# Kernel optimization log

Measured on AMD Instinct MI355X. Metric: run time of the kernel, lower is better.

## Reference

```python
import jax, jax.numpy as jnp
import numpy as np

V, E, L, H, B, T = 32000, 1024, 6, 16, 4, 1024
HS = E // H
FF = 4 * E


def setup_inputs() -> dict:
    key = jax.random.key(0)
    ks = jax.random.split(key, 16)
    s = 0.02
    n = lambda k, shp: jax.random.normal(k, shp, jnp.float32) * s
    return {
        "tokens": jax.random.randint(ks[0], (B, T), 0, V),
        "tok_emb": n(ks[1], (V, E)),
        "pos_emb": n(ks[2], (T, E)),
        "Wq": n(ks[3], (L, E, E)),
        "Wk": n(ks[4], (L, E, E)),
        "Wv": n(ks[5], (L, E, E)),
        "Wo": n(ks[6], (L, E, E)),
        "ln1_g": jnp.ones((L, E), jnp.float32),
        "ln1_b": jnp.zeros((L, E), jnp.float32),
        "W1": n(ks[7], (L, E, FF)),
        "b1": jnp.zeros((L, FF), jnp.float32),
        "W2": n(ks[8], (L, FF, E)),
        "b2": jnp.zeros((L, E), jnp.float32),
        "ln2_g": jnp.ones((L, E), jnp.float32),
        "ln2_b": jnp.zeros((L, E), jnp.float32),
        "lmh_w": n(ks[9], (E, V)),
        "lmh_b": jnp.zeros((V,), jnp.float32),
    }


def _layernorm(x, g, b):
    m = jnp.mean(x, axis=-1, keepdims=True)
    v = jnp.var(x, axis=-1, keepdims=True)
    return (x - m) * jax.lax.rsqrt(v + 1e-5) * g + b


def _forward(tokens, tok_emb, pos_emb, Wq, Wk, Wv, Wo, ln1_g, ln1_b,
             W1, b1, W2, b2, ln2_g, ln2_b, lmh_w, lmh_b):
    Bb, Tt = tokens.shape
    x = tok_emb[tokens] + pos_emb[:Tt]  # [B,T,E]
    mask = jnp.tril(jnp.ones((Tt, Tt), bool))  # causal
    scale = jnp.float32(E) ** -0.5  # NOTE: original scales by emb_dim, not head_size

    def block(x, p):
        wq, wk, wv, wo, g1, be1, w1, bb1, w2, bb2, g2, be2 = p
        h = _layernorm(x, g1, be1)
        q = (h @ wq).reshape(Bb, Tt, H, HS)
        k = (h @ wk).reshape(Bb, Tt, H, HS)
        v = (h @ wv).reshape(Bb, Tt, H, HS)
        scores = jnp.einsum('bqhd,bkhd->bhqk', q, k) * scale
        scores = jnp.where(mask, scores, -jnp.inf)
        w = jax.nn.softmax(scores, axis=-1)
        attn = jnp.einsum('bhqk,bkhd->bqhd', w, v).reshape(Bb, Tt, E)
        x = x + attn @ wo
        h2 = _layernorm(x, g2, be2)
        x = x + jax.nn.relu(h2 @ w1 + bb1) @ w2 + bb2
        return x, None

    x, _ = jax.lax.scan(block, x, (Wq, Wk, Wv, Wo, ln1_g, ln1_b,
                                   W1, b1, W2, b2, ln2_g, ln2_b))
    logits = x @ lmh_w + lmh_b  # [B,T,V]
    return logits


def reference(tokens, tok_emb, pos_emb, Wq, Wk, Wv, Wo, ln1_g, ln1_b,
              W1, b1, W2, b2, ln2_g, ln2_b, lmh_w, lmh_b):
    return _forward(tokens, tok_emb, pos_emb, Wq, Wk, Wv, Wo, ln1_g, ln1_b,
                    W1, b1, W2, b2, ln2_g, ln2_b, lmh_w, lmh_b)
```

## Files before the change

kernel.cpp:

```cpp
#include <hip/hip_runtime.h>
#include <cstdint>
#include <cstddef>

typedef __bf16 bf16;
typedef __attribute__((ext_vector_type(8))) __bf16 bf16x8;
typedef __attribute__((ext_vector_type(4))) float f32x4;

constexpr int kV = 32000, kE = 1024, kL = 6, kH = 16, kB = 4, kT = 1024;
constexpr int kHS = 64, kFF = 4096;
constexpr int kM = kB * kT;
constexpr float kScale = 0.03125f;
constexpr float kQScale = 0.0451038961f;

typedef __attribute__((address_space(1))) void gv_t;
typedef __attribute__((address_space(3))) void lv_t;

__device__ inline void gload_lds16(const void* g, void* l) {
  __builtin_amdgcn_global_load_lds((gv_t*)g, (lv_t*)l, 16, 0, 0);
}

#define SB0() __builtin_amdgcn_sched_barrier(0)
#define LGK0() asm volatile("s_waitcnt lgkmcnt(0)" ::: "memory")

enum { EPI_BF16 = 0, EPI_BF16_BIAS_RELU = 1, EPI_F32 = 2, EPI_F32_RES = 3, EPI_F32_BIAS = 4 };

__device__ inline void xcd_swz(int& bx, int& by) {
  int gx = gridDim.x, gy = gridDim.y;
  int nxy = gx * gy;
  int orig = by * gx + bx;
  int q = nxy >> 3, r = nxy & 7, xcd = orig & 7, idx = orig >> 3;
  int logical = (xcd < r ? xcd * (q + 1) : r * (q + 1) + (xcd - r) * q) + idx;
  bx = logical / gy;
  by = logical % gy;
}

template <int EPI>
__global__ __launch_bounds__(512, 2) void gemm256_k(
    const bf16* __restrict__ Ag, const bf16* __restrict__ Bg, void* Cg,
    const float* __restrict__ bias, const float* __restrict__ resid,
    int K, long lda, long ldb, long ldc) {
  extern __shared__ bf16 lds[];
  constexpr int SL = 8192;
  bf16* As = lds;
  bf16* Bs = lds + 4 * SL;

  const int tid = threadIdx.x, lane = tid & 63, w = tid >> 6;
  int bx = blockIdx.x, by = blockIdx.y;
  xcd_swz(bx, by);
  const long tm = (long)by * 256, tn = (long)bx * 256;
  const int wr = w >> 2, wc = w & 3;
  const int lr = lane & 15, kg = lane >> 4;

  const int p0 = tid, p1 = 512 + tid;
  const int r0 = p0 >> 2, ls0 = (p0 & 3) ^ ((r0 >> 1) & 3);
  const int r1 = p1 >> 2, ls1 = (p1 & 3) ^ ((r1 >> 1) & 3);
  const bf16* a0 = Ag + (tm + r0) * lda + ls0 * 8;
  const bf16* a1 = Ag + (tm + r1) * lda + ls1 * 8;
  const bf16* b0 = Bg + (tn + r0) * ldb + ls0 * 8;
  const bf16* b1 = Bg + (tn + r1) * ldb + ls1 * 8;
  const int wb = w * 1024;

  auto stage = [&](int s) {
    const int slot = s & 3;
    const long k0 = (long)s * 32;
    char* Ab = (char*)As + slot * (SL * 2);
    char* Bb = (char*)Bs + slot * (SL * 2);
    gload_lds16(a0 + k0, Ab + wb);
    gload_lds16(a1 + k0, Ab + 8192 + wb);
    gload_lds16(b0 + k0, Bb + wb);
    gload_lds16(b1 + k0, Bb + 8192 + wb);
  };

  int aoff[8], boff[4];
#pragma unroll
  for (int mi = 0; mi < 8; mi++) {
    int ar = wr * 128 + mi * 16 + lr;
    aoff[mi] = ar * 64 + ((kg ^ ((ar >> 1) & 3)) << 4);
  }
#pragma unroll
  for (int ni = 0; ni < 4; ni++) {
    int br = wc * 64 + ni * 16 + lr;
    boff[ni] = br * 64 + ((kg ^ ((br >> 1) & 3)) << 4);
  }

  f32x4 acc[8][4] = {};
  stage(0);
  stage(1);
  stage(2);
  const int NS = K >> 5;
  for (int s = 0; s < NS; s++) {
    SB0();
    if (s <= NS - 3)
      asm volatile("s_waitcnt vmcnt(8)" ::: "memory");
    else if (s == NS - 2)
      asm volatile("s_waitcnt vmcnt(4)" ::: "memory");
    else
      asm volatile("s_waitcnt vmcnt(0)" ::: "memory");
    __builtin_amdgcn_s_barrier();
    SB0();
    if (s + 3 < NS) stage(s + 3);
    const char* Ab = (const char*)As + (s & 3) * (SL * 2);
    const char* Bb = (const char*)Bs + (s & 3) * (SL * 2);
    bf16x8 af[8], bfr[4];
#pragma unroll
    for (int mi = 0; mi < 8; mi++) af[mi] = *(const bf16x8*)(Ab + aoff[mi]);
#pragma unroll
    for (int ni = 0; ni < 4; ni++) bfr[ni] = *(const bf16x8*)(Bb + boff[ni]);
    __builtin_amdgcn_s_setprio(1);
#pragma unroll
    for (int mi = 0; mi < 8; mi++)
#pragma unroll
      for (int ni = 0; ni < 4; ni++)
        acc[mi][ni] =
            __builtin_amdgcn_mfma_f32_16x16x32_bf16(af[mi], bfr[ni], acc[mi][ni], 0, 0, 0);
    __builtin_amdgcn_s_setprio(0);
  }

#pragma unroll
  for (int mi = 0; mi < 8; mi++) {
#pragma unroll
    for (int ni = 0; ni < 4; ni++) {
      const long rr = tm + wr * 128 + mi * 16 + kg * 4;
      const long cc = tn + wc * 64 + ni * 16 + lr;
      float bi = 0.f;
      if constexpr (EPI == EPI_BF16_BIAS_RELU || EPI == EPI_F32_BIAS) bi = bias[cc];
      if constexpr (EPI == EPI_F32_RES) bi = bias ? bias[cc] : 0.f;
#pragma unroll
      for (int j = 0; j < 4; j++) {
        long off = (rr + j) * ldc + cc;
        float val = acc[mi][ni][j];
        if constexpr (EPI == EPI_BF16)
          __builtin_nontemporal_store((bf16)val, &((bf16*)Cg)[off]);
        else if constexpr (EPI == EPI_BF16_BIAS_RELU)
          __builtin_nontemporal_store((bf16)fmaxf(val + bi, 0.f), &((bf16*)Cg)[off]);
        else if constexpr (EPI == EPI_F32)
          __builtin_nontemporal_store(val, &((float*)Cg)[off]);
        else if constexpr (EPI == EPI_F32_RES)
          ((float*)Cg)[off] = resid[off] + val + bi;
        else
          __builtin_nontemporal_store(val + bi, &((float*)Cg)[off]);
      }
    }
  }
}

template <int EPI>
__global__ __launch_bounds__(256, 2) void ring128_k(
    const bf16* __restrict__ Ag, const bf16* __restrict__ Bg, void* Cg,
    const float* __restrict__ bias, const float* __restrict__ resid,
    int K, long lda, long ldb, long ldc) {
  extern __shared__ bf16 lds[];
  char* Lb = (char*)lds;
  const int tid = threadIdx.x, lane = tid & 63, w = tid >> 6;
  int bx = blockIdx.x, by = blockIdx.y;
  xcd_swz(bx, by);
  const long tm = (long)by * 128, tn = (long)bx * 128;
  const int wr = w >> 1, wc = w & 1;
  const int lr = lane & 15, kg = lane >> 4;

  const int r0 = tid >> 2, g0 = (tid & 3) ^ ((r0 >> 1) & 3);
  const int r1 = (256 + tid) >> 2, g1 = ((256 + tid) & 3) ^ ((r1 >> 1) & 3);
  const bf16* a0 = Ag + (tm + r0) * lda + g0 * 8;
  const bf16* a1 = Ag + (tm + r1) * lda + g1 * 8;
  const bf16* b0 = Bg + (tn + r0) * ldb + g0 * 8;
  const bf16* b1 = Bg + (tn + r1) * ldb + g1 * 8;
  const int wb = w * 1024;

  auto stage = [&](int s) {
    const int slot = s & 3;
    const long k0 = (long)s * 32;
    char* Ab = Lb + slot * 16384;
    char* Bb = Ab + 8192;
    gload_lds16(a0 + k0, Ab + wb);
    gload_lds16(a1 + k0, Ab + 4096 + wb);
    gload_lds16(b0 + k0, Bb + wb);
    gload_lds16(b1 + k0, Bb + 4096 + wb);
  };

  int aoff[4], boff[4];
#pragma unroll
  for (int mi = 0; mi < 4; mi++) {
    int ar = wr * 64 + mi * 16 + lr;
    aoff[mi] = ar * 64 + ((kg ^ ((ar >> 1) & 3)) << 4);
  }
#pragma unroll
  for (int ni = 0; ni < 4; ni++) {
    int br = wc * 64 + ni * 16 + lr;
    boff[ni] = br * 64 + ((kg ^ ((br >> 1) & 3)) << 4);
  }

  f32x4 acc[4][4] = {};
  stage(0);
  stage(1);
  stage(2);
  const int NS = K >> 5;
  for (int s = 0; s < NS; s++) {
    SB0();
    if (s <= NS - 3)
      asm volatile("s_waitcnt vmcnt(8)" ::: "memory");
    else if (s == NS - 2)
      asm volatile("s_waitcnt vmcnt(4)" ::: "memory");
    else
      asm volatile("s_waitcnt vmcnt(0)" ::: "memory");
    __builtin_amdgcn_s_barrier();
    SB0();
    if (s + 3 < NS) stage(s + 3);
    const char* Ab = Lb + (s & 3) * 16384;
    const char* Bb = Ab + 8192;
    bf16x8 af[4], bfr[4];
#pragma unroll
    for (int mi = 0; mi < 4; mi++) af[mi] = *(const bf16x8*)(Ab + aoff[mi]);
#pragma unroll
    for (int ni = 0; ni < 4; ni++) bfr[ni] = *(const bf16x8*)(Bb + boff[ni]);
    __builtin_amdgcn_s_setprio(1);
#pragma unroll
    for (int mi = 0; mi < 4; mi++)
#pragma unroll
      for (int ni = 0; ni < 4; ni++)
        acc[mi][ni] =
            __builtin_amdgcn_mfma_f32_16x16x32_bf16(af[mi], bfr[ni], acc[mi][ni], 0, 0, 0);
    __builtin_amdgcn_s_setprio(0);
  }

#pragma unroll
  for (int mi = 0; mi < 4; mi++) {
#pragma unroll
    for (int ni = 0; ni < 4; ni++) {
      const long rr = tm + wr * 64 + mi * 16 + kg * 4;
      const long cc = tn + wc * 64 + ni * 16 + lr;
      float bi = 0.f;
      if constexpr (EPI == EPI_BF16_BIAS_RELU || EPI == EPI_F32_BIAS) bi = bias[cc];
      if constexpr (EPI == EPI_F32_RES) bi = bias ? bias[cc] : 0.f;
#pragma unroll
      for (int j = 0; j < 4; j++) {
        long off = (rr + j) * ldc + cc;
        float val = acc[mi][ni][j];
        if constexpr (EPI == EPI_BF16)
          ((bf16*)Cg)[off] = (bf16)val;
        else if constexpr (EPI == EPI_BF16_BIAS_RELU)
          ((bf16*)Cg)[off] = (bf16)fmaxf(val + bi, 0.f);
        else if constexpr (EPI == EPI_F32)
          ((float*)Cg)[off] = val;
        else if constexpr (EPI == EPI_F32_RES)
          ((float*)Cg)[off] = resid[off] + val + bi;
        else
          ((float*)Cg)[off] = val + bi;
      }
    }
  }
}

__global__ __launch_bounds__(128) void fa_k(const bf16* __restrict__ qkv,
                                            const bf16* __restrict__ vtG,
                                            bf16* __restrict__ out) {
  extern __shared__ bf16 lds[];
  char* L = (char*)lds;
  const int tid = threadIdx.x, lane = tid & 63, wq = tid >> 6;
  const int lr = lane & 15, kg = lane >> 4;
  const int bh = blockIdx.x, z = blockIdx.y;
  const int b = bh >> 4, hh = bh & 15;
  const long bq = (long)b * kT;
  const int qt = z < 4 ? z : 11 - z;
  const int q0 = qt * 128;
  const bf16* qbase = qkv + (bq + q0) * 3072 + hh * 64;
  const bf16* vbase = vtG + (long)bh * 64 * kT;

#pragma unroll
  for (int i = 0; i < 8; i++) {
    int p = i * 128 + tid;
    int row = p >> 3, s = p & 7;
    gload_lds16(qbase + (long)row * 3072 + ((s ^ (row & 7)) * 8),
                L + (i * 128 + (tid & ~63)) * 16);
  }
  auto stageKV = [&](int buf, int t) {
    const bf16* kb = qkv + (bq + t * 64) * 3072 + 1024 + hh * 64;
    const bf16* vb = vbase + t * 64;
#pragma unroll
    for (int i = 0; i < 4; i++) {
      int p = i * 128 + tid;
      int key = p >> 3, s = p & 7;
      gload_lds16(kb + (long)key * 3072 + ((s ^ (key & 7)) * 8),
                  L + 16384 + buf * 8192 + (i * 128 + (tid & ~63)) * 16);
    }
#pragma unroll
    for (int i = 0; i < 4; i++) {
      int p = i * 128 + tid;
      int key = p >> 3, s = p & 7;
      gload_lds16(vb + (long)key * kT + s * 8,
                  L + 32768 + buf * 8192 + (i * 128 + (tid & ~63)) * 16);
    }
  };
  stageKV(0, 0);
  __syncthreads();

  bf16x8 qf[4][2];
#pragma unroll
  for (int qi = 0; qi < 4; qi++)
#pragma unroll
    for (int ks = 0; ks < 2; ks++) {
      int qr = wq * 64 + qi * 16 + lr;
      bf16x8 v = *(const bf16x8*)(L + qr * 128 + ((ks * 64 + kg * 16) ^ ((qr & 7) << 4)));
#pragma unroll
      for (int e = 0; e < 8; e++) v[e] = (bf16)((float)v[e] * kQScale);
      qf[qi][ks] = v;
    }

  f32x4 O[4][4] = {};
  float lrun[4] = {0.f, 0.f, 0.f, 0.f};
  char* Pw = L + 49152 + wq * 9216;

  const int nt = 2 * qt + 2;
  int cur = 0;
  for (int t = 0; t < nt; t++) {
    if (t + 1 < nt) stageKV(cur ^ 1, t + 1);

    const char* Kb = L + 16384 + cur * 8192;
    f32x4 S[4][4] = {};
#pragma unroll
    for (int ks = 0; ks < 2; ks++) {
      bf16x8 kf[4];
#pragma unroll
      for (int ki = 0; ki < 4; ki++) {
        int key = ki * 16 + lr;
        kf[ki] = *(const bf16x8*)(Kb + key * 128 + ((ks * 64 + kg * 16) ^ ((key & 7) << 4)));
      }
#pragma unroll
      for (int ki = 0; ki < 4; ki++)
#pragma unroll
        for (int qi = 0; qi < 4; qi++)
          S[ki][qi] =
              __builtin_amdgcn_mfma_f32_16x16x32_bf16(kf[ki], qf[qi][ks], S[ki][qi], 0, 0, 0);
    }

    const int kvb = t * 64;
#pragma unroll
    for (int qi = 0; qi < 4; qi++) {
      const int q = q0 + wq * 64 + qi * 16 + lr;
      float ls = 0.f;
#pragma unroll
      for (int ki = 0; ki < 4; ki++) {
        union { bf16 h[4]; uint2 u; } pk;
#pragma unroll
        for (int j = 0; j < 4; j++) {
          int kv = kvb + ki * 16 + kg * 4 + j;
          float e = (kv <= q) ? exp2f(S[ki][qi][j]) : 0.f;
          ls += e;
          pk.h[j] = (bf16)e;
        }
        *(uint2*)(Pw + (qi * 16 + lr) * 144 + (ki * 16 + kg * 4) * 2) = pk.u;
      }
      ls += __shfl_xor(ls, 16);
      ls += __shfl_xor(ls, 32);
      lrun[qi] += ls;
    }
    LGK0();
    SB0();

    const char* Vb = L + 32768 + cur * 8192;
#pragma unroll
    for (int ks = 0; ks < 2; ks++) {
      bf16x8 pf[4], vf[4];
#pragma unroll
      for (int qi = 0; qi < 4; qi++)
        pf[qi] = *(const bf16x8*)(Pw + (qi * 16 + lr) * 144 + ks * 64 + kg * 16);
#pragma unroll
      for (int di = 0; di < 4; di++) {
        int d = di * 16 + lr;
        vf[di] = *(const bf16x8*)(Vb + d * 128 + ((ks * 64 + kg * 16) ^ ((d & 7) << 4)));
      }
#pragma unroll
      for (int qi = 0; qi < 4; qi++)
#pragma unroll
        for (int di = 0; di < 4; di++)
          O[qi][di] =
              __builtin_amdgcn_mfma_f32_16x16x32_bf16(pf[qi], vf[di], O[qi][di], 0, 0, 0);
    }
    __syncthreads();
    cur ^= 1;
  }

#pragma unroll
  for (int qi = 0; qi < 4; qi++) {
#pragma unroll
    for (int j = 0; j < 4; j++) {
      float lv = __shfl(lrun[qi], kg * 4 + j);
      float inv = 1.f / lv;
      long grow = bq + q0 + wq * 64 + qi * 16 + kg * 4 + j;
#pragma unroll
      for (int di = 0; di < 4; di++)
        out[grow * kE + hh * 64 + di * 16 + lr] = (bf16)(O[qi][di][j] * inv);
    }
  }
}

__global__ void vtrans_k(const bf16* __restrict__ qkv, bf16* __restrict__ vt) {
  __shared__ bf16 tbuf[32][33];
  int z = blockIdx.z;
  int b = z >> 4, h = z & 15;
  int t0 = blockIdx.x * 32, s0 = blockIdx.y * 32;
  int tx = threadIdx.x, ty = threadIdx.y;
#pragma unroll
  for (int i = 0; i < 32; i += 8)
    tbuf[ty + i][tx] = qkv[((long)b * kT + t0 + ty + i) * 3072 + 2048 + h * 64 + s0 + tx];
  __syncthreads();
#pragma unroll
  for (int i = 0; i < 32; i += 8) {
    int d = s0 + ty + i;
    int tt = t0 + tx;
    int g = (tt >> 3) & 7, e = tt & 7;
    long idx = ((long)z * 64 + d) * kT + (tt & ~63) + ((g ^ (d & 7)) << 3) + e;
    vt[idx] = tbuf[tx][ty + i];
  }
}

__global__ void tcvt_k(const float* __restrict__ in, bf16* __restrict__ out, int K, int N,
                       long in_zs, long out_zs) {
  __shared__ float t[64][33];
  long z = blockIdx.z;
  in += z * in_zs;
  out += z * out_zs;
  int n0 = blockIdx.x * 32, k0 = blockIdx.y * 64;
  int tid = threadIdx.y * 32 + threadIdx.x;
  int tx = threadIdx.x, ty = threadIdx.y;
#pragma unroll
  for (int i = 0; i < 8; i++) t[ty + i * 8][tx] = in[(long)(k0 + ty + i * 8) * N + n0 + tx];
  __syncthreads();
#pragma unroll
  for (int it = 0; it < 2; it++) {
    int q = it * 256 + tid;
    int r = q >> 4;
    int jj = q & 15;
    union { bf16 h[4]; uint2 u; } pk;
#pragma unroll
    for (int e = 0; e < 4; e++) pk.h[e] = (bf16)t[jj * 4 + e][r];
    *(uint2*)(out + (long)(n0 + r) * K + k0 + jj * 4) = pk.u;
  }
}

__global__ void embed_k(const int* __restrict__ toks, const float* __restrict__ te,
                        const float* __restrict__ pe, float* __restrict__ x) {
  int row = blockIdx.x, tid = threadIdx.x;
  int t = row & (kT - 1);
  long tok = toks[row];
  float4 a = ((const float4*)(te + tok * kE))[tid];
  float4 p = ((const float4*)(pe + (long)t * kE))[tid];
  float4 r{a.x + p.x, a.y + p.y, a.z + p.z, a.w + p.w};
  ((float4*)(x + (long)row * kE))[tid] = r;
}

__global__ void ln_k(const float* __restrict__ x, const float* __restrict__ g,
                     const float* __restrict__ b, bf16* __restrict__ h) {
  int row = blockIdx.x, tid = threadIdx.x, lane = tid & 63, w = tid >> 6;
  const float4 v = ((const float4*)(x + (long)row * kE))[tid];
  float s = v.x + v.y + v.z + v.w;
  float ss = v.x * v.x + v.y * v.y + v.z * v.z + v.w * v.w;
#pragma unroll
  for (int o = 32; o; o >>= 1) {
    s += __shfl_xor(s, o);
    ss += __shfl_xor(ss, o);
  }
  __shared__ float r1[4], r2[4];
  if (lane == 0) { r1[w] = s; r2[w] = ss; }
  __syncthreads();
  s = r1[0] + r1[1] + r1[2] + r1[3];
  ss = r2[0] + r2[1] + r2[2] + r2[3];
  float mean = s * (1.f / kE);
  float var = ss * (1.f / kE) - mean * mean;
  float rs = rsqrtf(var + 1e-5f);
  float4 gg = ((const float4*)g)[tid];
  float4 bb = ((const float4*)b)[tid];
  union { bf16 o[4]; uint2 u; } pk;
  pk.o[0] = (bf16)((v.x - mean) * rs * gg.x + bb.x);
  pk.o[1] = (bf16)((v.y - mean) * rs * gg.y + bb.y);
  pk.o[2] = (bf16)((v.z - mean) * rs * gg.z + bb.z);
  pk.o[3] = (bf16)((v.w - mean) * rs * gg.w + bb.w);
  ((uint2*)(h + (long)row * kE))[tid] = pk.u;
}

__global__ void cast_k(const float* __restrict__ x, bf16* __restrict__ o) {
  long i = (long)blockIdx.x * 256 + threadIdx.x;
  float4 v = ((const float4*)x)[i];
  union { bf16 b[4]; uint2 u; } pk;
  pk.b[0] = (bf16)v.x;
  pk.b[1] = (bf16)v.y;
  pk.b[2] = (bf16)v.z;
  pk.b[3] = (bf16)v.w;
  ((uint2*)o)[i] = pk.u;
}

extern "C" void kernel_launch(void* const* d_in, const int* in_sizes, int n_in,
                              void* d_out, int out_size, void* d_ws, size_t ws_size,
                              hipStream_t stream) {
  const int* toks = (const int*)d_in[0];
  const float* te = (const float*)d_in[1];
  const float* pe = (const float*)d_in[2];
  const float* Wq = (const float*)d_in[3];
  const float* Wk = (const float*)d_in[4];
  const float* Wv = (const float*)d_in[5];
  const float* Wo = (const float*)d_in[6];
  const float* g1 = (const float*)d_in[7];
  const float* be1 = (const float*)d_in[8];
  const float* W1 = (const float*)d_in[9];
  const float* bb1 = (const float*)d_in[10];
  const float* W2 = (const float*)d_in[11];
  const float* bb2 = (const float*)d_in[12];
  const float* g2 = (const float*)d_in[13];
  const float* be2 = (const float*)d_in[14];
  const float* lmw = (const float*)d_in[15];
  const float* lmb = (const float*)d_in[16];

  hipFuncSetAttribute(reinterpret_cast<const void*>(&gemm256_k<EPI_BF16>),
                      hipFuncAttributeMaxDynamicSharedMemorySize, 131072);
  hipFuncSetAttribute(reinterpret_cast<const void*>(&gemm256_k<EPI_BF16_BIAS_RELU>),
                      hipFuncAttributeMaxDynamicSharedMemorySize, 131072);
  hipFuncSetAttribute(reinterpret_cast<const void*>(&gemm256_k<EPI_F32_BIAS>),
                      hipFuncAttributeMaxDynamicSharedMemorySize, 131072);
  hipFuncSetAttribute(reinterpret_cast<const void*>(&ring128_k<EPI_F32_RES>),
                      hipFuncAttributeMaxDynamicSharedMemorySize, 65536);
  hipFuncSetAttribute(reinterpret_cast<const void*>(&fa_k),
                      hipFuncAttributeMaxDynamicSharedMemorySize, 67584);

  char* ws = (char*)d_ws;
  size_t off = 0;
  auto alloc = [&](size_t bytes) -> char* {
    char* p = ws + off;
    off += (bytes + 255) & ~(size_t)255;
    return p;
  };
  bf16* WqkvT = (bf16*)alloc((size_t)kL * 3 * kE * kE * 2);
  bf16* WoT = (bf16*)alloc((size_t)kL * kE * kE * 2);
  bf16* W1T = (bf16*)alloc((size_t)kL * kE * kFF * 2);
  bf16* W2T = (bf16*)alloc((size_t)kL * kE * kFF * 2);
  bf16* lmT = (bf16*)alloc((size_t)kV * kE * 2);
  float* x = (float*)alloc((size_t)kM * kE * 4);
  bf16* h = (bf16*)alloc((size_t)kM * kE * 2);
  bf16* qkv = (bf16*)alloc((size_t)kM * 3 * kE * 2);
  bf16* at = (bf16*)alloc((size_t)kM * kE * 2);
  bf16* vtG = (bf16*)alloc((size_t)kB * kH * 64 * kT * 2);

  bf16* mid = (bf16*)d_out;

  const long EE = (long)kE * kE;
  dim3 tb(32, 8);
  tcvt_k<<<dim3(kE / 32, kE / 64, kL), tb, 0, stream>>>(Wq, WqkvT, kE, kE, EE, 3 * EE);
  tcvt_k<<<dim3(kE / 32, kE / 64, kL), tb, 0, stream>>>(Wk, WqkvT + EE, kE, kE, EE, 3 * EE);
  tcvt_k<<<dim3(kE / 32, kE / 64, kL), tb, 0, stream>>>(Wv, WqkvT + 2 * EE, kE, kE, EE, 3 * EE);
  tcvt_k<<<dim3(kE / 32, kE / 64, kL), tb, 0, stream>>>(Wo, WoT, kE, kE, EE, EE);
  tcvt_k<<<dim3(kFF / 32, kE / 64, kL), tb, 0, stream>>>(W1, W1T, kE, kFF, 4 * EE, 4 * EE);
  tcvt_k<<<dim3(kE / 32, kFF / 64, kL), tb, 0, stream>>>(W2, W2T, kFF, kE, 4 * EE, 4 * EE);
  tcvt_k<<<dim3(kV / 32, kE / 64, 1), tb, 0, stream>>>(lmw, lmT, kE, kV, 0, 0);

  embed_k<<<kM, 256, 0, stream>>>(toks, te, pe, x);

  for (int l = 0; l < kL; l++) {
    ln_k<<<kM, 256, 0, stream>>>(x, g1 + l * kE, be1 + l * kE, h);
    gemm256_k<EPI_BF16><<<dim3(3 * kE / 256, kM / 256), 512, 131072, stream>>>(
        h, WqkvT + (size_t)l * 3 * EE, qkv, nullptr, nullptr, kE, kE, kE, 3 * kE);
    vtrans_k<<<dim3(kT / 32, kHS / 32, kB * kH), tb, 0, stream>>>(qkv, vtG);
    fa_k<<<dim3(kB * kH, 8), 128, 67584, stream>>>(qkv, vtG, at);
    ring128_k<EPI_F32_RES><<<dim3(kE / 128, kM / 128), 256, 65536, stream>>>(
        at, WoT + (size_t)l * EE, x, nullptr, x, kE, kE, kE, kE);
    ln_k<<<kM, 256, 0, stream>>>(x, g2 + l * kE, be2 + l * kE, h);
    gemm256_k<EPI_BF16_BIAS_RELU><<<dim3(kFF / 256, kM / 256), 512, 131072, stream>>>(
        h, W1T + (size_t)l * (size_t)kFF * kE, mid, bb1 + l * kFF, nullptr, kE, kE, kE, kFF);
    ring128_k<EPI_F32_RES><<<dim3(kE / 128, kM / 128), 256, 65536, stream>>>(
        mid, W2T + (size_t)l * (size_t)kE * kFF, x, bb2 + l * kE, x, kFF, kFF, kFF, kE);
  }
  cast_k<<<kM * kE / 1024, 256, 0, stream>>>(x, h);
  gemm256_k<EPI_F32_BIAS><<<dim3(kV / 256, kM / 256), 512, 131072, stream>>>(
      h, lmT, d_out, lmb, nullptr, kE, kE, kE, kV);
}
```

Before: 2.129 ms.

## Split-K the FFN down-projection into four partials with a separate reduction kernel

The W2 GEMM is launched with a z-dimension of four, each slice covering a quarter of K and writing fp32 partials into scratch space in the output buffer. A new reduce kernel sums the partials, adds the bias and accumulates into the residual stream. This raises grid parallelism for the long-K GEMM, at the cost of extra partial-sum memory traffic and an additional launch. The 256-tile GEMM epilogue also switches from nontemporal to regular stores.

```diff
diff --git a/kernel.cpp b/kernel.cpp
--- a/kernel.cpp
+++ b/kernel.cpp
@@ -130,15 +130,15 @@
         long off = (rr + j) * ldc + cc;
         float val = acc[mi][ni][j];
         if constexpr (EPI == EPI_BF16)
-          __builtin_nontemporal_store((bf16)val, &((bf16*)Cg)[off]);
+          ((bf16*)Cg)[off] = (bf16)val;
         else if constexpr (EPI == EPI_BF16_BIAS_RELU)
-          __builtin_nontemporal_store((bf16)fmaxf(val + bi, 0.f), &((bf16*)Cg)[off]);
+          ((bf16*)Cg)[off] = (bf16)fmaxf(val + bi, 0.f);
         else if constexpr (EPI == EPI_F32)
-          __builtin_nontemporal_store(val, &((float*)Cg)[off]);
+          ((float*)Cg)[off] = val;
         else if constexpr (EPI == EPI_F32_RES)
           ((float*)Cg)[off] = resid[off] + val + bi;
         else
-          __builtin_nontemporal_store(val + bi, &((float*)Cg)[off]);
+          ((float*)Cg)[off] = val + bi;
       }
     }
   }
@@ -148,12 +148,16 @@
 __global__ __launch_bounds__(256, 2) void ring128_k(
     const bf16* __restrict__ Ag, const bf16* __restrict__ Bg, void* Cg,
     const float* __restrict__ bias, const float* __restrict__ resid,
-    int K, long lda, long ldb, long ldc) {
+    int K, long lda, long ldb, long ldc, long sAz, long sBz, long sCz) {
   extern __shared__ bf16 lds[];
   char* Lb = (char*)lds;
   const int tid = threadIdx.x, lane = tid & 63, w = tid >> 6;
   int bx = blockIdx.x, by = blockIdx.y;
   xcd_swz(bx, by);
+  const int z = blockIdx.z;
+  Ag += (long)z * sAz;
+  Bg += (long)z * sBz;
+  const long czoff = (long)z * sCz;
   const long tm = (long)by * 128, tn = (long)bx * 128;
   const int wr = w >> 1, wc = w & 1;
   const int lr = lane & 15, kg = lane >> 4;
@@ -233,7 +237,7 @@
       if constexpr (EPI == EPI_F32_RES) bi = bias ? bias[cc] : 0.f;
 #pragma unroll
       for (int j = 0; j < 4; j++) {
-        long off = (rr + j) * ldc + cc;
+        long off = czoff + (rr + j) * ldc + cc;
         float val = acc[mi][ni][j];
         if constexpr (EPI == EPI_BF16)
           ((bf16*)Cg)[off] = (bf16)val;
@@ -248,6 +252,23 @@
       }
     }
   }
+}
+
+__global__ void reduce4_k(const float* __restrict__ p, const float* __restrict__ bias,
+                          float* __restrict__ x) {
+  long i = (long)blockIdx.x * 256 + threadIdx.x;
+  constexpr long NP = (long)kM * kE / 4;
+  float4 a = ((const float4*)p)[i];
+  float4 b = ((const float4*)p)[i + NP];
+  float4 c = ((const float4*)p)[i + 2 * NP];
+  float4 d = ((const float4*)p)[i + 3 * NP];
+  float4 bb = ((const float4*)bias)[i & (kE / 4 - 1)];
+  float4 xv = ((float4*)x)[i];
+  xv.x += a.x + b.x + c.x + d.x + bb.x;
+  xv.y += a.y + b.y + c.y + d.y + bb.y;
+  xv.z += a.z + b.z + c.z + d.z + bb.z;
+  xv.w += a.w + b.w + c.w + d.w + bb.w;
+  ((float4*)x)[i] = xv;
 }
 
 __global__ __launch_bounds__(128) void fa_k(const bf16* __restrict__ qkv,
@@ -517,6 +538,8 @@
                       hipFuncAttributeMaxDynamicSharedMemorySize, 131072);
   hipFuncSetAttribute(reinterpret_cast<const void*>(&ring128_k<EPI_F32_RES>),
                       hipFuncAttributeMaxDynamicSharedMemorySize, 65536);
+  hipFuncSetAttribute(reinterpret_cast<const void*>(&ring128_k<EPI_F32>),
+                      hipFuncAttributeMaxDynamicSharedMemorySize, 65536);
   hipFuncSetAttribute(reinterpret_cast<const void*>(&fa_k),
                       hipFuncAttributeMaxDynamicSharedMemorySize, 67584);
 
@@ -539,6 +562,7 @@
   bf16* vtG = (bf16*)alloc((size_t)kB * kH * 64 * kT * 2);
 
   bf16* mid = (bf16*)d_out;
+  float* pbuf = (float*)((char*)d_out + (64ull << 20));
 
   const long EE = (long)kE * kE;
   dim3 tb(32, 8);
@@ -558,13 +582,15 @@
         h, WqkvT + (size_t)l * 3 * EE, qkv, nullptr, nullptr, kE, kE, kE, 3 * kE);
     vtrans_k<<<dim3(kT / 32, kHS / 32, kB * kH), tb, 0, stream>>>(qkv, vtG);
     fa_k<<<dim3(kB * kH, 8), 128, 67584, stream>>>(qkv, vtG, at);
-    ring128_k<EPI_F32_RES><<<dim3(kE / 128, kM / 128), 256, 65536, stream>>>(
-        at, WoT + (size_t)l * EE, x, nullptr, x, kE, kE, kE, kE);
+    ring128_k<EPI_F32_RES><<<dim3(kE / 128, kM / 128, 1), 256, 65536, stream>>>(
+        at, WoT + (size_t)l * EE, x, nullptr, x, kE, kE, kE, kE, 0, 0, 0);
     ln_k<<<kM, 256, 0, stream>>>(x, g2 + l * kE, be2 + l * kE, h);
     gemm256_k<EPI_BF16_BIAS_RELU><<<dim3(kFF / 256, kM / 256), 512, 131072, stream>>>(
         h, W1T + (size_t)l * (size_t)kFF * kE, mid, bb1 + l * kFF, nullptr, kE, kE, kE, kFF);
-    ring128_k<EPI_F32_RES><<<dim3(kE / 128, kM / 128), 256, 65536, stream>>>(
-        mid, W2T + (size_t)l * (size_t)kE * kFF, x, bb2 + l * kE, x, kFF, kFF, kFF, kE);
+    ring128_k<EPI_F32><<<dim3(kE / 128, kM / 128, 4), 256, 65536, stream>>>(
+        mid, W2T + (size_t)l * (size_t)kE * kFF, pbuf, nullptr, nullptr, kFF / 4, kFF, kFF,
+        kE, kFF / 4, kFF / 4, (long)kM * kE);
+    reduce4_k<<<kM * kE / 1024, 256, 0, stream>>>(pbuf, bb2 + l * kE, x);
   }
   cast_k<<<kM * kE / 1024, 256, 0, stream>>>(x, h);
   gemm256_k<EPI_F32_BIAS><<<dim3(kV / 256, kM / 256), 512, 131072, stream>>>(
```

Measured after the change: 1.996 ms. 1.07x faster.

## Generalize ring GEMM to templated tiles with 3-slot pipeline and use it for QKV/FFN

Applied to the files above, without the earlier changes.

Replaces the 4-slot ring128 kernel with a templated ring3 kernel using a 3-deep LDS ring (prefetch distance 2) and 3 blocks per CU. The QKV and FFN-up GEMMs now use 128x128 tiles with 256 threads in place of the 256x256 gemm256 kernel, and the Wo/W2 residual GEMMs use 128x64 tiles to double the grid. The gemm256 epilogue also drops nontemporal stores. The aim is more occupancy and better wave balance across CUs, at the cost of less reuse per tile and a shallower prefetch pipeline.

```diff
diff --git a/kernel.cpp b/kernel.cpp
--- a/kernel.cpp
+++ b/kernel.cpp
@@ -9,7 +9,6 @@
 constexpr int kV = 32000, kE = 1024, kL = 6, kH = 16, kB = 4, kT = 1024;
 constexpr int kHS = 64, kFF = 4096;
 constexpr int kM = kB * kT;
-constexpr float kScale = 0.03125f;
 constexpr float kQScale = 0.0451038961f;
 
 typedef __attribute__((address_space(1))) void gv_t;
@@ -130,91 +129,106 @@
         long off = (rr + j) * ldc + cc;
         float val = acc[mi][ni][j];
         if constexpr (EPI == EPI_BF16)
-          __builtin_nontemporal_store((bf16)val, &((bf16*)Cg)[off]);
+          ((bf16*)Cg)[off] = (bf16)val;
         else if constexpr (EPI == EPI_BF16_BIAS_RELU)
-          __builtin_nontemporal_store((bf16)fmaxf(val + bi, 0.f), &((bf16*)Cg)[off]);
+          ((bf16*)Cg)[off] = (bf16)fmaxf(val + bi, 0.f);
         else if constexpr (EPI == EPI_F32)
-          __builtin_nontemporal_store(val, &((float*)Cg)[off]);
+          ((float*)Cg)[off] = val;
         else if constexpr (EPI == EPI_F32_RES)
           ((float*)Cg)[off] = resid[off] + val + bi;
         else
-          __builtin_nontemporal_store(val + bi, &((float*)Cg)[off]);
+          ((float*)Cg)[off] = val + bi;
       }
     }
   }
 }
 
-template <int EPI>
-__global__ __launch_bounds__(256, 2) void ring128_k(
+template <int BM, int BN, int EPI>
+__global__ __launch_bounds__(256, 3) void ring3_k(
     const bf16* __restrict__ Ag, const bf16* __restrict__ Bg, void* Cg,
     const float* __restrict__ bias, const float* __restrict__ resid,
     int K, long lda, long ldb, long ldc) {
   extern __shared__ bf16 lds[];
   char* Lb = (char*)lds;
+  constexpr int A_IT = BM * 4 / 256;
+  constexpr int B_IT = BN * 4 / 256;
+  constexpr int L = A_IT + B_IT;
+  constexpr int SLOT = (BM + BN) * 64;
+  constexpr int NWN = BN / 64, NWM = 4 / NWN, WM = BM / NWM;
+  constexpr int MI = WM / 16;
+
   const int tid = threadIdx.x, lane = tid & 63, w = tid >> 6;
   int bx = blockIdx.x, by = blockIdx.y;
   xcd_swz(bx, by);
-  const long tm = (long)by * 128, tn = (long)bx * 128;
-  const int wr = w >> 1, wc = w & 1;
+  const long tm = (long)by * BM, tn = (long)bx * BN;
+  const int wr = w / NWN, wc = w % NWN;
+  const int wm0 = wr * WM, wn0 = wc * 64;
   const int lr = lane & 15, kg = lane >> 4;
 
-  const int r0 = tid >> 2, g0 = (tid & 3) ^ ((r0 >> 1) & 3);
-  const int r1 = (256 + tid) >> 2, g1 = ((256 + tid) & 3) ^ ((r1 >> 1) & 3);
-  const bf16* a0 = Ag + (tm + r0) * lda + g0 * 8;
-  const bf16* a1 = Ag + (tm + r1) * lda + g1 * 8;
-  const bf16* b0 = Bg + (tn + r0) * ldb + g0 * 8;
-  const bf16* b1 = Bg + (tn + r1) * ldb + g1 * 8;
-  const int wb = w * 1024;
+  const bf16* aSrc[A_IT];
+  const bf16* bSrc[B_IT];
+#pragma unroll
+  for (int i = 0; i < A_IT; i++) {
+    int p = i * 256 + tid;
+    int row = p >> 2, g = (p & 3) ^ ((row >> 1) & 3);
+    aSrc[i] = Ag + (tm + row) * lda + g * 8;
+  }
+#pragma unroll
+  for (int i = 0; i < B_IT; i++) {
+    int p = i * 256 + tid;
+    int row = p >> 2, g = (p & 3) ^ ((row >> 1) & 3);
+    bSrc[i] = Bg + (tn + row) * ldb + g * 8;
+  }
+  const int wdst = (tid & ~63) * 16;
 
   auto stage = [&](int s) {
-    const int slot = s & 3;
+    char* Ab = Lb + (s % 3) * SLOT;
+    char* Bb = Ab + BM * 64;
     const long k0 = (long)s * 32;
-    char* Ab = Lb + slot * 16384;
-    char* Bb = Ab + 8192;
-    gload_lds16(a0 + k0, Ab + wb);
-    gload_lds16(a1 + k0, Ab + 4096 + wb);
-    gload_lds16(b0 + k0, Bb + wb);
-    gload_lds16(b1 + k0, Bb + 4096 + wb);
+#pragma unroll
+    for (int i = 0; i < A_IT; i++) gload_lds16(aSrc[i] + k0, Ab + i * 4096 + wdst);
+#pragma unroll
+    for (int i = 0; i < B_IT; i++) gload_lds16(bSrc[i] + k0, Bb + i * 4096 + wdst);
   };
 
-  int aoff[4], boff[4];
-#pragma unroll
-  for (int mi = 0; mi < 4; mi++) {
-    int ar = wr * 64 + mi * 16 + lr;
+  int aoff[MI], boff[4];
+#pragma unroll
+  for (int mi = 0; mi < MI; mi++) {
+    int ar = wm0 + mi * 16 + lr;
     aoff[mi] = ar * 64 + ((kg ^ ((ar >> 1) & 3)) << 4);
   }
 #pragma unroll
   for (int ni = 0; ni < 4; ni++) {
-    int br = wc * 64 + ni * 16 + lr;
-    boff[ni] = br * 64 + ((kg ^ ((br >> 1) & 3)) << 4);
-  }
-
-  f32x4 acc[4][4] = {};
+    int br = wn0 + ni * 16 + lr;
+    boff[ni] = BM * 64 + br * 64 + ((kg ^ ((br >> 1) & 3)) << 4);
+  }
+
+  f32x4 acc[MI][4] = {};
   stage(0);
   stage(1);
-  stage(2);
   const int NS = K >> 5;
   for (int s = 0; s < NS; s++) {
     SB0();
-    if (s <= NS - 3)
-      asm volatile("s_waitcnt vmcnt(8)" ::: "memory");
-    else if (s == NS - 2)
-      asm volatile("s_waitcnt vmcnt(4)" ::: "memory");
-    else
+    if (s + 1 < NS) {
+      if constexpr (L == 4)
+        asm volatile("s_waitcnt vmcnt(4)" ::: "memory");
+      else
+        asm volatile("s_waitcnt vmcnt(3)" ::: "memory");
+    } else {
       asm volatile("s_waitcnt vmcnt(0)" ::: "memory");
+    }
     __builtin_amdgcn_s_barrier();
     SB0();
-    if (s + 3 < NS) stage(s + 3);
-    const char* Ab = Lb + (s & 3) * 16384;
-    const char* Bb = Ab + 8192;
-    bf16x8 af[4], bfr[4];
-#pragma unroll
-    for (int mi = 0; mi < 4; mi++) af[mi] = *(const bf16x8*)(Ab + aoff[mi]);
-#pragma unroll
-    for (int ni = 0; ni < 4; ni++) bfr[ni] = *(const bf16x8*)(Bb + boff[ni]);
+    if (s + 2 < NS) stage(s + 2);
+    const char* Sb = Lb + (s % 3) * SLOT;
+    bf16x8 af[MI], bfr[4];
+#pragma unroll
+    for (int mi = 0; mi < MI; mi++) af[mi] = *(const bf16x8*)(Sb + aoff[mi]);
+#pragma unroll
+    for (int ni = 0; ni < 4; ni++) bfr[ni] = *(const bf16x8*)(Sb + boff[ni]);
     __builtin_amdgcn_s_setprio(1);
 #pragma unroll
-    for (int mi = 0; mi < 4; mi++)
+    for (int mi = 0; mi < MI; mi++)
 #pragma unroll
       for (int ni = 0; ni < 4; ni++)
         acc[mi][ni] =
@@ -223,11 +237,11 @@
   }
 
 #pragma unroll
-  for (int mi = 0; mi < 4; mi++) {
+  for (int mi = 0; mi < MI; mi++) {
 #pragma unroll
     for (int ni = 0; ni < 4; ni++) {
-      const long rr = tm + wr * 64 + mi * 16 + kg * 4;
-      const long cc = tn + wc * 64 + ni * 16 + lr;
+      const long rr = tm + wm0 + mi * 16 + kg * 4;
+      const long cc = tn + wn0 + ni * 16 + lr;
       float bi = 0.f;
       if constexpr (EPI == EPI_BF16_BIAS_RELU || EPI == EPI_F32_BIAS) bi = bias[cc];
       if constexpr (EPI == EPI_F32_RES) bi = bias ? bias[cc] : 0.f;
@@ -509,14 +523,14 @@
   const float* lmw = (const float*)d_in[15];
   const float* lmb = (const float*)d_in[16];
 
-  hipFuncSetAttribute(reinterpret_cast<const void*>(&gemm256_k<EPI_BF16>),
-                      hipFuncAttributeMaxDynamicSharedMemorySize, 131072);
-  hipFuncSetAttribute(reinterpret_cast<const void*>(&gemm256_k<EPI_BF16_BIAS_RELU>),
-                      hipFuncAttributeMaxDynamicSharedMemorySize, 131072);
   hipFuncSetAttribute(reinterpret_cast<const void*>(&gemm256_k<EPI_F32_BIAS>),
                       hipFuncAttributeMaxDynamicSharedMemorySize, 131072);
-  hipFuncSetAttribute(reinterpret_cast<const void*>(&ring128_k<EPI_F32_RES>),
-                      hipFuncAttributeMaxDynamicSharedMemorySize, 65536);
+  hipFuncSetAttribute(reinterpret_cast<const void*>(&ring3_k<128, 128, EPI_BF16>),
+                      hipFuncAttributeMaxDynamicSharedMemorySize, 49152);
+  hipFuncSetAttribute(reinterpret_cast<const void*>(&ring3_k<128, 128, EPI_BF16_BIAS_RELU>),
+                      hipFuncAttributeMaxDynamicSharedMemorySize, 49152);
+  hipFuncSetAttribute(reinterpret_cast<const void*>(&ring3_k<128, 64, EPI_F32_RES>),
+                      hipFuncAttributeMaxDynamicSharedMemorySize, 36864);
   hipFuncSetAttribute(reinterpret_cast<const void*>(&fa_k),
                       hipFuncAttributeMaxDynamicSharedMemorySize, 67584);
 
@@ -554,16 +568,16 @@
 
   for (int l = 0; l < kL; l++) {
     ln_k<<<kM, 256, 0, stream>>>(x, g1 + l * kE, be1 + l * kE, h);
-    gemm256_k<EPI_BF16><<<dim3(3 * kE / 256, kM / 256), 512, 131072, stream>>>(
+    ring3_k<128, 128, EPI_BF16><<<dim3(3 * kE / 128, kM / 128), 256, 49152, stream>>>(
         h, WqkvT + (size_t)l * 3 * EE, qkv, nullptr, nullptr, kE, kE, kE, 3 * kE);
     vtrans_k<<<dim3(kT / 32, kHS / 32, kB * kH), tb, 0, stream>>>(qkv, vtG);
     fa_k<<<dim3(kB * kH, 8), 128, 67584, stream>>>(qkv, vtG, at);
-    ring128_k<EPI_F32_RES><<<dim3(kE / 128, kM / 128), 256, 65536, stream>>>(
+    ring3_k<128, 64, EPI_F32_RES><<<dim3(kE / 64, kM / 128), 256, 36864, stream>>>(
         at, WoT + (size_t)l * EE, x, nullptr, x, kE, kE, kE, kE);
     ln_k<<<kM, 256, 0, stream>>>(x, g2 + l * kE, be2 + l * kE, h);
-    gemm256_k<EPI_BF16_BIAS_RELU><<<dim3(kFF / 256, kM / 256), 512, 131072, stream>>>(
+    ring3_k<128, 128, EPI_BF16_BIAS_RELU><<<dim3(kFF / 128, kM / 128), 256, 49152, stream>>>(
         h, W1T + (size_t)l * (size_t)kFF * kE, mid, bb1 + l * kFF, nullptr, kE, kE, kE, kFF);
-    ring128_k<EPI_F32_RES><<<dim3(kE / 128, kM / 128), 256, 65536, stream>>>(
+    ring3_k<128, 64, EPI_F32_RES><<<dim3(kE / 64, kM / 128), 256, 36864, stream>>>(
         mid, W2T + (size_t)l * (size_t)kE * kFF, x, bb2 + l * kE, x, kFF, kFF, kFF, kE);
   }
   cast_k<<<kM * kE / 1024, 256, 0, stream>>>(x, h);
```

Result: faster. 2.018 ms (-5.2%).
